# Kernel optimization log

Measured on AMD Instinct MI355X. Metric: run time of the kernel, lower is better.

Reference implementation:

```python
import jax, jax.numpy as jnp
import numpy as np

# ---- static config (from grid_conf / data_aug_conf) ----
B, N, C = 4, 6, 64            # batch, cameras, camC
OGH, OGW = 256, 704           # final_dim
DOWN = 16                     # 32 // up_scale
FH, FW = OGH // DOWN, OGW // DOWN   # 16, 44
DB0, DB1, DBS = 4.0, 45.0, 1.0      # dbound
D = int((DB1 - DB0) / DBS)          # 41 depth bins
DX = np.array([0.5, 0.5, 20.0], np.float32)            # dx
BX = np.array([-49.75, -49.75, 0.0], np.float32)        # bx (lower + dx/2)
NX = (200, 200, 1)                                       # nx


def make_frustum():
    # [D, FH, FW, 3] pixel (u, v, depth) frustum, matches torch create_frustum
    ds = jnp.arange(DB0, DB1, DBS, dtype=jnp.float32)[:, None, None] * jnp.ones((1, FH, FW), jnp.float32)
    xs = jnp.linspace(0.0, OGW - 1.0, FW, dtype=jnp.float32)[None, None, :] * jnp.ones((D, FH, 1), jnp.float32)
    ys = jnp.linspace(0.0, OGH - 1.0, FH, dtype=jnp.float32)[None, :, None] * jnp.ones((D, 1, FW), jnp.float32)
    return jnp.stack([xs, ys, ds], axis=-1)


def get_geometry(rots, trans, intrins, post_rots, post_trans):
    # frustum points -> ego frame, [B, N, D, FH, FW, 3]
    pts = make_frustum()[None, None] - post_trans[:, :, None, None, None, :]
    pts = jnp.einsum('bnij,bndhwj->bndhwi', jnp.linalg.inv(post_rots), pts)
    # un-project: (u*d, v*d, d)
    pts = jnp.concatenate([pts[..., :2] * pts[..., 2:3], pts[..., 2:3]], axis=-1)
    combine = rots @ jnp.linalg.inv(intrins)
    return jnp.einsum('bnij,bndhwj->bndhwi', combine, pts) + trans[:, :, None, None, None, :]


def voxel_pooling(geom, x):
    # geom: [B,N,D,H,W,3] ego coords; x: [B,N,D,H,W,C] lifted features
    dx = jnp.asarray(DX); bx = jnp.asarray(BX)
    # voxel indices; .astype(int32) truncates toward zero like torch .long()
    gi = ((geom - (bx - dx / 2.0)) / dx).astype(jnp.int32)
    Np = B * N * D * FH * FW
    gi = gi.reshape(Np, 3)
    xf = x.reshape(Np, C)
    bidx = jnp.repeat(jnp.arange(B, dtype=jnp.int32), N * D * FH * FW)
    valid = ((gi[:, 0] >= 0) & (gi[:, 0] < NX[0]) &
             (gi[:, 1] >= 0) & (gi[:, 1] < NX[1]) &
             (gi[:, 2] >= 0) & (gi[:, 2] < NX[2]))
    # flat voxel id: (((b*nz + z)*nx0 + xi)*nx1 + yi)
    flat = ((bidx * NX[2] + gi[:, 2]) * NX[0] + gi[:, 0]) * NX[1] + gi[:, 1]
    flat = jnp.where(valid, flat, 0)
    xf = xf * valid[:, None].astype(xf.dtype)
    nvox = B * NX[2] * NX[0] * NX[1]
    # scatter-add == sort + cumsum-trick per-voxel sum in the torch code
    final = jax.ops.segment_sum(xf, flat, num_segments=nvox)          # [nvox, C]
    final = final.reshape(B, NX[2], NX[0], NX[1], C)
    final = jnp.transpose(final, (0, 1, 4, 2, 3)).reshape(B, NX[2] * C, NX[0], NX[1])
    return final


def setup_inputs() -> dict:
    key = jax.random.key(0)
    k1, k2 = jax.random.split(key)
    feat_depth = jax.random.normal(k1, (B, N, D, FH, FW), jnp.float32)
    feat_pv = jax.random.normal(k2, (B, N, C, FH, FW), jnp.float32)
    # realistic 6-camera nuScenes-like rig, intrinsics scaled to 704x256
    base = np.array([[0., 0., 1.], [-1., 0., 0.], [0., -1., 0.]], np.float32)  # cam axes -> ego axes
    rots = np.zeros((B, N, 3, 3), np.float32)
    trans = np.zeros((B, N, 3), np.float32)
    for n in range(N):
        yaw = 2.0 * np.pi * n / N
        Rz = np.array([[np.cos(yaw), -np.sin(yaw), 0.], [np.sin(yaw), np.cos(yaw), 0.], [0., 0., 1.]], np.float32)
        rots[:, n] = Rz @ base
        trans[:, n] = Rz @ np.array([1.5, 0.0, 1.6], np.float32)
    fx = 1266.0 * (OGW / 1600.0)
    intr = np.array([[fx, 0., OGW / 2.0], [0., fx, OGH / 2.0], [0., 0., 1.]], np.float32)
    return {
        'feat_depth': feat_depth,
        'feat_pv': feat_pv,
        'rots': jnp.asarray(rots),
        'trans': jnp.asarray(trans),
        'intrins': jnp.asarray(np.broadcast_to(intr, (B, N, 3, 3)).copy()),
        'post_rots': jnp.asarray(np.broadcast_to(np.eye(3, dtype=np.float32), (B, N, 3, 3)).copy()),
        'post_trans': jnp.zeros((B, N, 3), jnp.float32),
    }


def reference(feat_depth, feat_pv, rots, trans, intrins, post_rots, post_trans):
    geom = get_geometry(rots, trans, intrins, post_rots, post_trans)
    geom = jax.lax.stop_gradient(geom)  # torch casts to .long(): indices are non-diff
    depth = jax.nn.softmax(feat_depth, axis=2)                 # get_depth_dist over D
    # lift: depth.unsqueeze(1) * feat.unsqueeze(2) -> [B,N,D,C,H,W] -> [B,N,D,H,W,C]
    x = depth[:, :, :, None] * feat_pv[:, :, None]
    x = jnp.transpose(x, (0, 1, 2, 4, 5, 3))
    return voxel_pooling(geom, x)                               # [B, C*nz, 200, 200]
```

## Files before the change

kernel.cpp:

```cpp
#include <hip/hip_runtime.h>
#include <math.h>

namespace {
constexpr int kB = 4, kN = 6, kC = 64, kD = 41, kFH = 16, kFW = 44;
constexpr int kNX0 = 200, kNX1 = 200;
constexpr int kHW  = kFH * kFW;
constexpr int kPix = kB * kN * kHW;
constexpr int kPts = kPix * kD;
constexpr int kVox = kB * kNX0 * kNX1;
constexpr int kPvElems = kPix * kC;
constexpr int kScanBlks = kVox / 256;
constexpr int kPvtTiles = kPix / 64;
constexpr int kSmBlks = kPix / 256;
constexpr int kGeoBlks = kPts / 256;
constexpr int kFrontBlks = kPvtTiles + kSmBlks + kGeoBlks;

constexpr size_t kOffPvT    = 0;
constexpr size_t kSzPvT     = (size_t)kPvElems * 4;
constexpr size_t kOffVox    = kOffPvT + kSzPvT;
constexpr size_t kSzVox     = (size_t)kPts * 4;
constexpr size_t kOffWgt    = kOffVox + kSzVox;
constexpr size_t kSzWgt     = (size_t)kPts * 4;
constexpr size_t kOffCnt    = kOffWgt + kSzWgt;
constexpr size_t kSzCnt     = (size_t)kVox * 4;
constexpr size_t kOffOffs   = kOffCnt + kSzCnt;
constexpr size_t kSzOffs    = 640256;
constexpr size_t kOffBSum   = kOffOffs + kSzOffs;
constexpr size_t kSzBSum    = 2560;
constexpr size_t kOffSKW    = kOffBSum + kSzBSum;
constexpr size_t kSzSKW     = (size_t)kPts * 8;
constexpr size_t kWsNeed    = kOffSKW + kSzSKW + 256;

constexpr int kZeroVec4 = (int)(kSzCnt / 16);
constexpr int kZeroBlks = (kZeroVec4 + 255) / 256;
}

__device__ __forceinline__ void inv3x3(const float m[9], float inv[9]) {
    float a = m[0], b = m[1], c = m[2];
    float d = m[3], e = m[4], f = m[5];
    float g = m[6], h = m[7], i = m[8];
    float A =  (e * i - f * h);
    float Bm = -(d * i - f * g);
    float Cm =  (d * h - e * g);
    float det = a * A + b * Bm + c * Cm;
    float r = 1.0f / det;
    inv[0] = A * r;
    inv[1] = -(b * i - c * h) * r;
    inv[2] =  (b * f - c * e) * r;
    inv[3] = Bm * r;
    inv[4] =  (a * i - c * g) * r;
    inv[5] = -(a * f - c * d) * r;
    inv[6] = Cm * r;
    inv[7] = -(a * h - b * g) * r;
    inv[8] =  (a * e - b * d) * r;
}

__device__ __forceinline__ int geo_flat(int q,
                                        const float* __restrict__ rots,
                                        const float* __restrict__ trans,
                                        const float* __restrict__ intrins,
                                        const float* __restrict__ post_rots,
                                        const float* __restrict__ post_trans) {
    const int bn  = q / (kD * kHW);
    const int rem = q - bn * (kD * kHW);
    const int d   = rem / kHW;
    const int hw  = rem - d * kHW;
    const int h   = hw / kFW;
    const int w   = hw - h * kFW;
    const int b   = bn / kN;

    const float* R  = rots       + bn * 9;
    const float* K  = intrins    + bn * 9;
    const float* PR = post_rots  + bn * 9;
    const float* PT = post_trans + bn * 3;
    const float* T  = trans      + bn * 3;

    float Km[9], PRm[9];
#pragma unroll
    for (int i = 0; i < 9; ++i) { Km[i] = K[i]; PRm[i] = PR[i]; }
    float invK[9], invPR[9];
    inv3x3(Km, invK);
    inv3x3(PRm, invPR);
    float M[9];
#pragma unroll
    for (int i = 0; i < 3; ++i)
#pragma unroll
        for (int j = 0; j < 3; ++j)
            M[i * 3 + j] = R[i * 3 + 0] * invK[0 * 3 + j]
                         + R[i * 3 + 1] * invK[1 * 3 + j]
                         + R[i * 3 + 2] * invK[2 * 3 + j];

    const float u  = (float)w * (703.0f / 43.0f);
    const float v  = (float)h * 17.0f;
    const float dv = 4.0f + (float)d;
    const float px = u - PT[0], py = v - PT[1], pz = dv - PT[2];
    const float ax = invPR[0] * px + invPR[1] * py + invPR[2] * pz;
    const float ay = invPR[3] * px + invPR[4] * py + invPR[5] * pz;
    const float az = invPR[6] * px + invPR[7] * py + invPR[8] * pz;
    const float qx = ax * az, qy = ay * az, qz = az;
    const float gx = M[0] * qx + M[1] * qy + M[2] * qz + T[0];
    const float gy = M[3] * qx + M[4] * qy + M[5] * qz + T[1];
    const float gz = M[6] * qx + M[7] * qy + M[8] * qz + T[2];
    const float fx = (gx + 50.0f) / 0.5f;
    const float fy = (gy + 50.0f) / 0.5f;
    const float fz = (gz + 10.0f) / 20.0f;
    const int gix = (int)fx;
    const int giy = (int)fy;
    const int giz = (int)fz;
    if (gix >= 0 && gix < kNX0 && giy >= 0 && giy < kNX1 && giz == 0)
        return (b * kNX0 + gix) * kNX1 + giy;
    return -1;
}

__global__ __launch_bounds__(256) void lss_zero(uint4* __restrict__ dst) {
    const int i = blockIdx.x * 256 + threadIdx.x;
    if (i < kZeroVec4) dst[i] = make_uint4(0u, 0u, 0u, 0u);
}

__global__ __launch_bounds__(256) void lss_front(
    const float* __restrict__ pv,
    const float* __restrict__ feat_depth,
    const float* __restrict__ rots,
    const float* __restrict__ trans,
    const float* __restrict__ intrins,
    const float* __restrict__ post_rots,
    const float* __restrict__ post_trans,
    float* __restrict__ pvT,
    float* __restrict__ wgtArr,
    int* __restrict__ voxArr,
    unsigned* __restrict__ counts)
{
    __shared__ float t[64][65];
    const int blk = blockIdx.x;
    const int tid = threadIdx.x;

    if (blk < kPvtTiles) {
        const int pix0 = blk * 64;
        const int bn  = pix0 / kHW;
        const int hw0 = pix0 - bn * kHW;
        const int lane = tid & 63;
        const int wv   = tid >> 6;
        const float* src = pv + (size_t)(bn * kC) * kHW + hw0;
#pragma unroll
        for (int cc = 0; cc < 16; ++cc) {
            const int c = wv * 16 + cc;
            t[c][lane] = src[(size_t)c * kHW + lane];
        }
        __syncthreads();
        float* dst = pvT + (size_t)pix0 * kC;
#pragma unroll
        for (int jj = 0; jj < 16; ++jj) {
            const int j = wv * 16 + jj;
            dst[j * kC + lane] = t[lane][j];
        }
    } else if (blk < kPvtTiles + kSmBlks) {
        const int pix = (blk - kPvtTiles) * 256 + tid;
        const int bn = pix / kHW;
        const int hw = pix - bn * kHW;
        const float* p = feat_depth + (size_t)(bn * kD) * kHW + hw;
        float v[kD];
#pragma unroll
        for (int d = 0; d < kD; ++d) v[d] = p[(size_t)d * kHW];
        float mx = v[0];
#pragma unroll
        for (int d = 1; d < kD; ++d) mx = fmaxf(mx, v[d]);
        float sm = 0.0f;
#pragma unroll
        for (int d = 0; d < kD; ++d) { v[d] = __expf(v[d] - mx); sm += v[d]; }
        const float inv = 1.0f / sm;
        float* o = wgtArr + (size_t)(bn * kD) * kHW + hw;
#pragma unroll
        for (int d = 0; d < kD; ++d) o[(size_t)d * kHW] = v[d] * inv;
    } else {
        const int q = (blk - kPvtTiles - kSmBlks) * 256 + tid;
        const int f = geo_flat(q, rots, trans, intrins, post_rots, post_trans);
        if (f >= 0) atomicAdd(&counts[f], 1u);
        voxArr[q] = f;
    }
}

__global__ __launch_bounds__(256) void lss_scan_a(const unsigned* __restrict__ counts,
                                                  unsigned* __restrict__ offsets,
                                                  unsigned* __restrict__ blockSums) {
    const int i = blockIdx.x * 256 + threadIdx.x;
    const int lane = threadIdx.x & 63;
    const int wv = threadIdx.x >> 6;
    const unsigned c = counts[i];
    unsigned s = c;
#pragma unroll
    for (int o = 1; o < 64; o <<= 1) {
        unsigned v = __shfl_up(s, o);
        if (lane >= o) s += v;
    }
    __shared__ unsigned wsum[4];
    if (lane == 63) wsum[wv] = s;
    __syncthreads();
    unsigned base = 0;
#pragma unroll
    for (int k = 0; k < 3; ++k)
        if (k < wv) base += wsum[k];
    const unsigned incl = s + base;
    offsets[i] = incl - c;
    if (threadIdx.x == 255) blockSums[blockIdx.x] = incl;
}

__global__ __launch_bounds__(1024) void lss_scan_b(unsigned* __restrict__ blockSums) {
    const int t = threadIdx.x;
    const int lane = t & 63;
    const int wv = t >> 6;
    const unsigned c = (t < kScanBlks) ? blockSums[t] : 0u;
    unsigned s = c;
#pragma unroll
    for (int o = 1; o < 64; o <<= 1) {
        unsigned v = __shfl_up(s, o);
        if (lane >= o) s += v;
    }
    __shared__ unsigned wsum[16];
    if (lane == 63) wsum[wv] = s;
    __syncthreads();
    unsigned base = 0;
#pragma unroll
    for (int k = 0; k < 15; ++k)
        if (k < wv) base += wsum[k];
    if (t < kScanBlks) blockSums[t] = (s + base) - c;
}

__global__ __launch_bounds__(256) void lss_order(const int* __restrict__ voxArr,
                                                 const float* __restrict__ wgtArr,
                                                 unsigned* __restrict__ offsets,
                                                 const unsigned* __restrict__ blockSums,
                                                 uint2* __restrict__ skw) {
    const int q = blockIdx.x * 256 + threadIdx.x;
    const int f = voxArr[q];
    if (f >= 0) {
        const unsigned slot = atomicAdd(&offsets[f], 1u) + blockSums[f >> 8];
        const int bn  = q / (kD * kHW);
        const int rem = q - bn * (kD * kHW);
        const int hw  = rem % kHW;
        uint2 u;
        u.x = (unsigned)(bn * kHW + hw);
        u.y = __float_as_uint(wgtArr[q]);
        skw[slot] = u;
    }
}

__global__ __launch_bounds__(512) void lss_gather(const float* __restrict__ pvT,
                                                  const unsigned* __restrict__ offsets,
                                                  const unsigned* __restrict__ blockSums,
                                                  const uint2* __restrict__ skw,
                                                  float* __restrict__ out) {
    constexpr int kChunk = 2048;
    __shared__ float acc[50][65];
    __shared__ uint2 sbuf[kChunk];
    __shared__ unsigned rowOff[51];
    const int tile = blockIdx.x;
    const int yt = tile & 3;
    const int xi = (tile >> 2) % kNX0;
    const int b  = tile / (kNX0 * 4);
    const int yi0 = yt * 50;
    const int lane = threadIdx.x & 63;
    const int wave = threadIdx.x >> 6;
    const int flat0 = (b * kNX0 + xi) * kNX1 + yi0;

    for (int e = threadIdx.x; e < 50 * 65; e += 512)
        ((float*)acc)[e] = 0.0f;
    if (threadIdx.x < 51) {
        const int f = flat0 - 1 + (int)threadIdx.x;
        rowOff[threadIdx.x] = (f < 0) ? 0u : (offsets[f] + blockSums[f >> 8]);
    }
    __syncthreads();

    const unsigned seg0 = rowOff[0];
    const unsigned seg1 = rowOff[50];

    for (unsigned cb = seg0; cb < seg1; cb += (unsigned)kChunk) {
        const unsigned ce = min(cb + (unsigned)kChunk, seg1);
        const int n = (int)(ce - cb);
        for (int e = threadIdx.x; e < n; e += 512)
            sbuf[e] = skw[cb + e];
        __syncthreads();

        for (int j = wave; j < 50; j += 8) {
            unsigned s0 = max(rowOff[j], cb);
            unsigned e0 = min(rowOff[j + 1], ce);
            if (s0 >= e0) continue;
            float a0 = 0.0f, a1 = 0.0f, a2 = 0.0f, a3 = 0.0f;
            int p  = (int)(s0 - cb);
            int pe = (int)(e0 - cb);
            for (; p + 8 <= pe; p += 8) {
                const uint2 u0 = sbuf[p + 0];
                const uint2 u1 = sbuf[p + 1];
                const uint2 u2 = sbuf[p + 2];
                const uint2 u3 = sbuf[p + 3];
                const uint2 u4 = sbuf[p + 4];
                const uint2 u5 = sbuf[p + 5];
                const uint2 u6 = sbuf[p + 6];
                const uint2 u7 = sbuf[p + 7];
                const float* r0 = pvT + (size_t)((unsigned)__builtin_amdgcn_readfirstlane(u0.x)) * kC;
                const float* r1 = pvT + (size_t)((unsigned)__builtin_amdgcn_readfirstlane(u1.x)) * kC;
                const float* r2 = pvT + (size_t)((unsigned)__builtin_amdgcn_readfirstlane(u2.x)) * kC;
                const float* r3 = pvT + (size_t)((unsigned)__builtin_amdgcn_readfirstlane(u3.x)) * kC;
                const float* r4 = pvT + (size_t)((unsigned)__builtin_amdgcn_readfirstlane(u4.x)) * kC;
                const float* r5 = pvT + (size_t)((unsigned)__builtin_amdgcn_readfirstlane(u5.x)) * kC;
                const float* r6 = pvT + (size_t)((unsigned)__builtin_amdgcn_readfirstlane(u6.x)) * kC;
                const float* r7 = pvT + (size_t)((unsigned)__builtin_amdgcn_readfirstlane(u7.x)) * kC;
                const float f0 = r0[lane], f1 = r1[lane], f2 = r2[lane], f3 = r3[lane];
                const float f4 = r4[lane], f5 = r5[lane], f6 = r6[lane], f7 = r7[lane];
                a0 = fmaf(__uint_as_float(__builtin_amdgcn_readfirstlane(u0.y)), f0, a0);
                a1 = fmaf(__uint_as_float(__builtin_amdgcn_readfirstlane(u1.y)), f1, a1);
                a2 = fmaf(__uint_as_float(__builtin_amdgcn_readfirstlane(u2.y)), f2, a2);
                a3 = fmaf(__uint_as_float(__builtin_amdgcn_readfirstlane(u3.y)), f3, a3);
                a0 = fmaf(__uint_as_float(__builtin_amdgcn_readfirstlane(u4.y)), f4, a0);
                a1 = fmaf(__uint_as_float(__builtin_amdgcn_readfirstlane(u5.y)), f5, a1);
                a2 = fmaf(__uint_as_float(__builtin_amdgcn_readfirstlane(u6.y)), f6, a2);
                a3 = fmaf(__uint_as_float(__builtin_amdgcn_readfirstlane(u7.y)), f7, a3);
            }
            for (; p < pe; ++p) {
                const uint2 u = sbuf[p];
                const float* r = pvT + (size_t)((unsigned)__builtin_amdgcn_readfirstlane(u.x)) * kC;
                a0 = fmaf(__uint_as_float(__builtin_amdgcn_readfirstlane(u.y)), r[lane], a0);
            }
            acc[j][lane] += (a0 + a1) + (a2 + a3);
        }
        __syncthreads();
    }
    __syncthreads();

    for (int e = threadIdx.x; e < kC * 50; e += 512) {
        const int c = e / 50, j = e % 50;
        out[((b * kC + c) * (kNX0 * kNX1)) + xi * kNX1 + yi0 + j] = acc[j][c];
    }
}

__global__ __launch_bounds__(256) void lss_scatter_fb(
    const float* __restrict__ feat_depth,
    const float* __restrict__ feat_pv,
    const float* __restrict__ rots,
    const float* __restrict__ trans,
    const float* __restrict__ intrins,
    const float* __restrict__ post_rots,
    const float* __restrict__ post_trans,
    float* __restrict__ out)
{
    const int lane = threadIdx.x & 63;
    const int wave = threadIdx.x >> 6;
    const int pix  = blockIdx.x * 4 + wave;
    const int w  = pix % kFW;
    const int h  = (pix / kFW) % kFH;
    const int bn = pix / kHW;
    const int b  = bn / kN;
    const int pixBase = h * kFW + w;
    float fd = -INFINITY;
    if (lane < kD)
        fd = feat_depth[(bn * kD + lane) * kHW + pixBase];
    float mx = fd;
#pragma unroll
    for (int off = 32; off >= 1; off >>= 1)
        mx = fmaxf(mx, __shfl_xor(mx, off));
    float ex = (lane < kD) ? __expf(fd - mx) : 0.0f;
    float sm = ex;
#pragma unroll
    for (int off = 32; off >= 1; off >>= 1)
        sm += __shfl_xor(sm, off);
    const float wgt = ex / sm;
    int vox = -1;
    if (lane < kD) {
        const int q = (bn * kD + lane) * kHW + pixBase;
        const int f = geo_flat(q, rots, trans, intrins, post_rots, post_trans);
        if (f >= 0) vox = f % (kNX0 * kNX1);
    }
    const float fc = feat_pv[(bn * kC + lane) * kHW + pixBase];
    const int outBase = (b * kC + lane) * (kNX0 * kNX1);
#pragma unroll 1
    for (int d = 0; d < kD; ++d) {
        const int   vd = __shfl(vox, d);
        const float wd = __shfl(wgt, d);
        if (vd >= 0)
            atomicAdd(&out[outBase + vd], wd * fc);
    }
}

extern "C" void kernel_launch(void* const* d_in, const int* in_sizes, int n_in,
                              void* d_out, int out_size, void* d_ws, size_t ws_size,
                              hipStream_t stream) {
    const float* feat_depth = (const float*)d_in[0];
    const float* feat_pv    = (const float*)d_in[1];
    const float* rots       = (const float*)d_in[2];
    const float* trans      = (const float*)d_in[3];
    const float* intrins    = (const float*)d_in[4];
    const float* post_rots  = (const float*)d_in[5];
    const float* post_trans = (const float*)d_in[6];
    float* out = (float*)d_out;

    if (ws_size < kWsNeed) {
        hipMemsetAsync(out, 0, (size_t)out_size * sizeof(float), stream);
        lss_scatter_fb<<<kPix / 4, 256, 0, stream>>>(
            feat_depth, feat_pv, rots, trans, intrins, post_rots, post_trans, out);
        return;
    }

    char* ws = (char*)d_ws;
    float*    pvT      = (float*)   (ws + kOffPvT);
    int*      voxArr   = (int*)     (ws + kOffVox);
    float*    wgtArr   = (float*)   (ws + kOffWgt);
    unsigned* counts   = (unsigned*)(ws + kOffCnt);
    unsigned* offsets  = (unsigned*)(ws + kOffOffs);
    unsigned* blockSums= (unsigned*)(ws + kOffBSum);
    uint2*    skw      = (uint2*)   (ws + kOffSKW);

    lss_zero<<<kZeroBlks, 256, 0, stream>>>((uint4*)(ws + kOffCnt));
    lss_front<<<kFrontBlks, 256, 0, stream>>>(
        feat_pv, feat_depth, rots, trans, intrins, post_rots, post_trans,
        pvT, wgtArr, voxArr, counts);
    lss_scan_a<<<kScanBlks, 256, 0, stream>>>(counts, offsets, blockSums);
    lss_scan_b<<<1, 1024, 0, stream>>>(blockSums);
    lss_order<<<kPts / 256, 256, 0, stream>>>(voxArr, wgtArr, offsets, blockSums, skw);
    lss_gather<<<kB * kNX0 * 4, 512, 0, stream>>>(pvT, offsets, blockSums, skw, out);
}
```

Measured before the change: 112.3 us.

## Fold block-sum scan into order and gather kernels, drop scan_b launch

Removes the single-block lss_scan_b kernel and instead has every block of lss_order and lss_gather redundantly scan the 625 block sums into shared memory before use. This eliminates one kernel launch and its serialization point in the pipeline. In exchange every block re-reads the block-sum array and runs an extra scan with two barriers, which adds work across the thousands of blocks of lss_order.

```diff
diff --git a/kernel.cpp b/kernel.cpp
--- a/kernel.cpp
+++ b/kernel.cpp
@@ -204,25 +204,38 @@
     if (threadIdx.x == 255) blockSums[blockIdx.x] = incl;
 }
 
-__global__ __launch_bounds__(1024) void lss_scan_b(unsigned* __restrict__ blockSums) {
-    const int t = threadIdx.x;
-    const int lane = t & 63;
-    const int wv = t >> 6;
-    const unsigned c = (t < kScanBlks) ? blockSums[t] : 0u;
-    unsigned s = c;
+template <int NT, int EPT, int NWAVE>
+__device__ __forceinline__ void scan_bases(const unsigned* __restrict__ blockSums,
+                                           unsigned* basesL, unsigned* wsum) {
+    const int tid  = threadIdx.x;
+    const int lane = tid & 63;
+    const int wv   = tid >> 6;
+    unsigned c[EPT];
+    unsigned t3 = 0;
+    const int lo = tid * EPT;
+#pragma unroll
+    for (int k = 0; k < EPT; ++k) {
+        c[k] = (lo + k < kScanBlks) ? blockSums[lo + k] : 0u;
+        t3 += c[k];
+    }
+    unsigned si = t3;
 #pragma unroll
     for (int o = 1; o < 64; o <<= 1) {
-        unsigned v = __shfl_up(s, o);
-        if (lane >= o) s += v;
-    }
-    __shared__ unsigned wsum[16];
-    if (lane == 63) wsum[wv] = s;
+        unsigned v = __shfl_up(si, o);
+        if (lane >= o) si += v;
+    }
+    if (lane == 63) wsum[wv] = si;
     __syncthreads();
-    unsigned base = 0;
-#pragma unroll
-    for (int k = 0; k < 15; ++k)
-        if (k < wv) base += wsum[k];
-    if (t < kScanBlks) blockSums[t] = (s + base) - c;
+    unsigned b2 = 0;
+#pragma unroll
+    for (int k = 0; k < NWAVE - 1; ++k)
+        if (k < wv) b2 += wsum[k];
+    unsigned run = si - t3 + b2;
+#pragma unroll
+    for (int k = 0; k < EPT; ++k) {
+        if (lo + k < kScanBlks) { basesL[lo + k] = run; run += c[k]; }
+    }
+    __syncthreads();
 }
 
 __global__ __launch_bounds__(256) void lss_order(const int* __restrict__ voxArr,
@@ -230,10 +243,14 @@
                                                  unsigned* __restrict__ offsets,
                                                  const unsigned* __restrict__ blockSums,
                                                  uint2* __restrict__ skw) {
+    __shared__ unsigned basesL[kScanBlks];
+    __shared__ unsigned wsum[4];
+    scan_bases<256, 3, 4>(blockSums, basesL, wsum);
+
     const int q = blockIdx.x * 256 + threadIdx.x;
     const int f = voxArr[q];
     if (f >= 0) {
-        const unsigned slot = atomicAdd(&offsets[f], 1u) + blockSums[f >> 8];
+        const unsigned slot = atomicAdd(&offsets[f], 1u) + basesL[f >> 8];
         const int bn  = q / (kD * kHW);
         const int rem = q - bn * (kD * kHW);
         const int hw  = rem % kHW;
@@ -253,6 +270,10 @@
     __shared__ float acc[50][65];
     __shared__ uint2 sbuf[kChunk];
     __shared__ unsigned rowOff[51];
+    __shared__ unsigned basesL[kScanBlks];
+    __shared__ unsigned wsum[8];
+    scan_bases<512, 2, 8>(blockSums, basesL, wsum);
+
     const int tile = blockIdx.x;
     const int yt = tile & 3;
     const int xi = (tile >> 2) % kNX0;
@@ -266,7 +287,7 @@
         ((float*)acc)[e] = 0.0f;
     if (threadIdx.x < 51) {
         const int f = flat0 - 1 + (int)threadIdx.x;
-        rowOff[threadIdx.x] = (f < 0) ? 0u : (offsets[f] + blockSums[f >> 8]);
+        rowOff[threadIdx.x] = (f < 0) ? 0u : (offsets[f] + basesL[f >> 8]);
     }
     __syncthreads();
 
@@ -413,7 +434,6 @@
         feat_pv, feat_depth, rots, trans, intrins, post_rots, post_trans,
         pvT, wgtArr, voxArr, counts);
     lss_scan_a<<<kScanBlks, 256, 0, stream>>>(counts, offsets, blockSums);
-    lss_scan_b<<<1, 1024, 0, stream>>>(blockSums);
     lss_order<<<kPts / 256, 256, 0, stream>>>(voxArr, wgtArr, offsets, blockSums, skw);
     lss_gather<<<kB * kNX0 * 4, 512, 0, stream>>>(pvT, offsets, blockSums, skw, out);
 }
```

After: 115.3 us. 1.03x slower.

## Balance gather work across waves by splitting chunk points evenly

Applied to the files above, without the earlier changes.

Rather than assigning each wave a fixed set of output voxel rows, which leaves waves idle when points are unevenly distributed across the 50 voxels, each wave now takes an equal contiguous slice of the chunk's sorted points. It binary-searches the starting voxel, walks the voxel boundaries while accumulating, and flushes partial sums into the LDS accumulator with atomicAdd. The aim is to remove load imbalance between waves. In exchange it adds LDS atomics, a per-point boundary check, and a single accumulator chain in place of four independent ones, which reduces FMA overlap.

```diff
diff --git a/kernel.cpp b/kernel.cpp
--- a/kernel.cpp
+++ b/kernel.cpp
@@ -280,47 +280,44 @@
             sbuf[e] = skw[cb + e];
         __syncthreads();
 
-        for (int j = wave; j < 50; j += 8) {
-            unsigned s0 = max(rowOff[j], cb);
-            unsigned e0 = min(rowOff[j + 1], ce);
-            if (s0 >= e0) continue;
-            float a0 = 0.0f, a1 = 0.0f, a2 = 0.0f, a3 = 0.0f;
-            int p  = (int)(s0 - cb);
-            int pe = (int)(e0 - cb);
-            for (; p + 8 <= pe; p += 8) {
-                const uint2 u0 = sbuf[p + 0];
-                const uint2 u1 = sbuf[p + 1];
-                const uint2 u2 = sbuf[p + 2];
-                const uint2 u3 = sbuf[p + 3];
-                const uint2 u4 = sbuf[p + 4];
-                const uint2 u5 = sbuf[p + 5];
-                const uint2 u6 = sbuf[p + 6];
-                const uint2 u7 = sbuf[p + 7];
-                const float* r0 = pvT + (size_t)((unsigned)__builtin_amdgcn_readfirstlane(u0.x)) * kC;
-                const float* r1 = pvT + (size_t)((unsigned)__builtin_amdgcn_readfirstlane(u1.x)) * kC;
-                const float* r2 = pvT + (size_t)((unsigned)__builtin_amdgcn_readfirstlane(u2.x)) * kC;
-                const float* r3 = pvT + (size_t)((unsigned)__builtin_amdgcn_readfirstlane(u3.x)) * kC;
-                const float* r4 = pvT + (size_t)((unsigned)__builtin_amdgcn_readfirstlane(u4.x)) * kC;
-                const float* r5 = pvT + (size_t)((unsigned)__builtin_amdgcn_readfirstlane(u5.x)) * kC;
-                const float* r6 = pvT + (size_t)((unsigned)__builtin_amdgcn_readfirstlane(u6.x)) * kC;
-                const float* r7 = pvT + (size_t)((unsigned)__builtin_amdgcn_readfirstlane(u7.x)) * kC;
-                const float f0 = r0[lane], f1 = r1[lane], f2 = r2[lane], f3 = r3[lane];
-                const float f4 = r4[lane], f5 = r5[lane], f6 = r6[lane], f7 = r7[lane];
-                a0 = fmaf(__uint_as_float(__builtin_amdgcn_readfirstlane(u0.y)), f0, a0);
-                a1 = fmaf(__uint_as_float(__builtin_amdgcn_readfirstlane(u1.y)), f1, a1);
-                a2 = fmaf(__uint_as_float(__builtin_amdgcn_readfirstlane(u2.y)), f2, a2);
-                a3 = fmaf(__uint_as_float(__builtin_amdgcn_readfirstlane(u3.y)), f3, a3);
-                a0 = fmaf(__uint_as_float(__builtin_amdgcn_readfirstlane(u4.y)), f4, a0);
-                a1 = fmaf(__uint_as_float(__builtin_amdgcn_readfirstlane(u5.y)), f5, a1);
-                a2 = fmaf(__uint_as_float(__builtin_amdgcn_readfirstlane(u6.y)), f6, a2);
-                a3 = fmaf(__uint_as_float(__builtin_amdgcn_readfirstlane(u7.y)), f7, a3);
+        const int spanLen = (n + 7) >> 3;
+        int p  = wave * spanLen;
+        int pe = min(p + spanLen, n);
+        if (p < pe) {
+            const unsigned gp0 = cb + (unsigned)p;
+            int lo = 0, hi = 50;
+            while (hi - lo > 1) {
+                const int mid = (lo + hi) >> 1;
+                if (rowOff[mid] <= gp0) lo = mid; else hi = mid;
             }
-            for (; p < pe; ++p) {
-                const uint2 u = sbuf[p];
-                const float* r = pvT + (size_t)((unsigned)__builtin_amdgcn_readfirstlane(u.x)) * kC;
-                a0 = fmaf(__uint_as_float(__builtin_amdgcn_readfirstlane(u.y)), r[lane], a0);
+            int j = lo;
+            float a = 0.0f;
+            while (p < pe) {
+                const int batch = min(8, pe - p);
+                uint2 u[8];
+                float f[8];
+#pragma unroll
+                for (int k = 0; k < 8; ++k)
+                    if (k < batch) u[k] = sbuf[p + k];
+#pragma unroll
+                for (int k = 0; k < 8; ++k)
+                    if (k < batch)
+                        f[k] = pvT[(size_t)((unsigned)__builtin_amdgcn_readfirstlane(u[k].x)) * kC + lane];
+#pragma unroll
+                for (int k = 0; k < 8; ++k) {
+                    if (k < batch) {
+                        const unsigned gp = cb + (unsigned)(p + k);
+                        while (gp >= rowOff[j + 1]) {
+                            if (a != 0.0f) atomicAdd(&acc[j][lane], a);
+                            a = 0.0f;
+                            ++j;
+                        }
+                        a = fmaf(__uint_as_float(__builtin_amdgcn_readfirstlane(u[k].y)), f[k], a);
+                    }
+                }
+                p += batch;
             }
-            acc[j][lane] += (a0 + a1) + (a2 + a3);
+            if (a != 0.0f) atomicAdd(&acc[j][lane], a);
         }
         __syncthreads();
     }
```

Result: slower. 150.2 us (+33.8%).
